# Kernel tuning notes

Hardware: AMD Instinct MI355X
Metric: run time of the kernel (lower is better)

Reference implementation:

```python
import jax, jax.numpy as jnp
import numpy as np

T, B, N_IN, N_HID, N_OUT = 32, 32, 512, 1024, 256

def _xavier(key, fan_in, fan_out):
    scale = jnp.sqrt(2.0 / (fan_in + fan_out)).astype(jnp.float32)
    return jax.random.normal(key, (fan_in, fan_out), dtype=jnp.float32) * scale

def setup_inputs() -> dict:
    key = jax.random.key(0)
    ks = jax.random.split(key, 8)
    return {
        'x_in': jax.random.normal(ks[0], (T, B, N_IN), dtype=jnp.float32),
        'W_i': _xavier(ks[1], N_IN, N_HID),
        'W_z': _xavier(ks[2], N_HID, N_HID),
        'W_c': _xavier(ks[3], N_HID, N_HID),
        'W_h': _xavier(ks[4], N_HID, N_HID),
        'W_ho': _xavier(ks[5], N_HID, N_HID),
        'W_o': _xavier(ks[6], N_HID, N_OUT),
        'lam': jnp.array([0.9], dtype=jnp.float32),
        'eta': jnp.array([0.5], dtype=jnp.float32),
        'g': jnp.ones((1, N_HID), dtype=jnp.float32),
        'b': jnp.ones((1, N_HID), dtype=jnp.float32),
        'mode': 0,
        'time': T,
    }

def reference(x_in, W_i, W_z, W_c, W_h, W_ho, W_o, lam, eta, g, b, mode, time):
    relu = jax.nn.relu
    n_steps = int(time)  # dt = 1.0
    batch, n_hidden = x_in.shape[1], W_i.shape[1]

    def step(carry, x_t):
        h, a = carry
        x = relu(x_t)                              # [B, n_in]
        s = relu(x @ W_i)                          # [B, H]
        z = relu(s @ W_z)                          # [B, H]
        zc = z @ W_c                               # reused twice
        h = relu(zc + h @ W_h)                     # [B, H]
        # fast-weight update: a <- lam*a + eta * h^T h (per-batch outer product)
        a = lam[0] * a + eta[0] * jnp.einsum('bi,bj->bij', h, h)  # [B, H, H]
        # one inner readout/normalization step
        hs = h @ W_h + zc + jnp.einsum('bk,bkj->bj', h, a)        # [B, H]
        mu = jnp.mean(hs, axis=0)                                 # [H]
        sig = jnp.sqrt(jnp.mean((hs - mu) ** 2, axis=0))          # [H] (biased std)
        hs = relu(g[0] * (hs - mu) / sig + b[0])
        return (hs, a), None

    h0 = jnp.zeros((batch, n_hidden), dtype=x_in.dtype)
    a0 = jnp.zeros((batch, n_hidden, n_hidden), dtype=x_in.dtype)
    (h, a), _ = jax.lax.scan(step, (h0, a0), x_in[:n_steps])

    o = relu(h @ W_ho)
    y = relu(o @ W_o)
    return y.reshape(1, batch, -1)
```

## Files before the change

### kernel.cpp

```cpp
#include <hip/hip_runtime.h>
#include <hip/hip_bf16.h>

#define T_   32
#define B_   32
#define NIN_ 512
#define H_   1024
#define NOUT_ 256
#define NBLK 64
#define NTHR 1024
#define NCOL 16
#define NSLOT 80
#define PACKB 128

typedef short bf16x8 __attribute__((ext_vector_type(8)));
typedef float f32x4  __attribute__((ext_vector_type(4)));
typedef unsigned int u32x4 __attribute__((ext_vector_type(4)));

__device__ __forceinline__ float bf2f(unsigned short u) {
  union { unsigned int i; float f; } x; x.i = ((unsigned int)u) << 16; return x.f;
}
__device__ __forceinline__ unsigned short f2bf(float f) {
  __hip_bfloat16 h = __float2bfloat16(f);
  return *reinterpret_cast<unsigned short*>(&h);
}
__device__ __forceinline__ unsigned int packf(float v) {
  unsigned short h = f2bf(v);
  unsigned short l = f2bf(v - bf2f(h));
  return ((unsigned int)h << 16) | l;
}
__device__ __forceinline__ void unpack8v(u32x4 a, u32x4 b, bf16x8& hi, bf16x8& lo) {
  unsigned int t[8] = {a[0], a[1], a[2], a[3], b[0], b[1], b[2], b[3]};
  union { bf16x8 v; unsigned int u[4]; } H, L;
#pragma unroll
  for (int j = 0; j < 4; j++) {
    unsigned int e = t[2 * j], o = t[2 * j + 1];
    H.u[j] = (o & 0xFFFF0000u) | (e >> 16);
    L.u[j] = (o << 16) | (e & 0xFFFFu);
  }
  hi = H.v; lo = L.v;
}

__device__ __forceinline__ void astu(unsigned int* p, unsigned int v) {
  __hip_atomic_store(p, v, __ATOMIC_RELAXED, __HIP_MEMORY_SCOPE_AGENT);
}
__device__ __forceinline__ void astf(float* p, float v) {
  __hip_atomic_store(p, v, __ATOMIC_RELAXED, __HIP_MEMORY_SCOPE_AGENT);
}
__device__ __forceinline__ void aaddf(float* p, float v) {
  __hip_atomic_fetch_add(p, v, __ATOMIC_RELAXED, __HIP_MEMORY_SCOPE_AGENT);
}

__device__ __forceinline__ void rendezvous(int* cnt, int slot) {
  __syncthreads();
  if (threadIdx.x == 0) {
    __hip_atomic_fetch_add(&cnt[slot], 1, __ATOMIC_RELAXED, __HIP_MEMORY_SCOPE_AGENT);
    while (__hip_atomic_load(&cnt[slot], __ATOMIC_RELAXED, __HIP_MEMORY_SCOPE_AGENT) < NBLK)
      __builtin_amdgcn_s_sleep(1);
    __atomic_signal_fence(__ATOMIC_ACQUIRE);
  }
  __syncthreads();
}

__global__ void init_detect(const unsigned short* __restrict__ x_raw,
                            int* __restrict__ flag, int* __restrict__ cnt) {
  __shared__ int bad;
  if (threadIdx.x == 0) bad = 0;
  __syncthreads();
  int c = 0;
  for (int i = threadIdx.x; i < 2048; i += 256) {
    float v = bf2f(x_raw[i]);
    if (!(fabsf(v) < 1e9f)) c++;
  }
  if (c) atomicAdd(&bad, 1);
  __syncthreads();
  if (threadIdx.x == 0) flag[0] = bad ? 1 : 0;
  for (int i = threadIdx.x; i < NSLOT; i += 256)
    __hip_atomic_store(&cnt[i], 0, __ATOMIC_RELAXED, __HIP_MEMORY_SCOPE_AGENT);
}

__global__ void prep_all(
    const void* __restrict__ x_in, unsigned int* __restrict__ X_pk,
    const void* lam, const void* eta, const void* g, const void* b,
    float* __restrict__ par,
    const void* __restrict__ W_i,  unsigned short* __restrict__ WiT_hi,  unsigned short* __restrict__ WiT_lo,
    const void* __restrict__ W_z,  unsigned short* __restrict__ WzT_hi,  unsigned short* __restrict__ WzT_lo,
    const void* __restrict__ W_c,  unsigned short* __restrict__ WcT_hi,  unsigned short* __restrict__ WcT_lo,
    const void* __restrict__ W_h,  unsigned short* __restrict__ WhT_hi,  unsigned short* __restrict__ WhT_lo,
    const void* __restrict__ W_ho, unsigned short* __restrict__ WhoT_hi, unsigned short* __restrict__ WhoT_lo,
    const void* __restrict__ W_o,  unsigned short* __restrict__ WoT_hi,  unsigned short* __restrict__ WoT_lo,
    const int* __restrict__ flag)
{
  const bool isf32 = flag[0] != 0;
  int blk = blockIdx.x;
  if (blk < PACKB) {
    const int n = T_ * B_ * NIN_;
    for (int i = blk * 256 + threadIdx.x; i < n; i += PACKB * 256) {
      float v = isf32 ? ((const float*)x_in)[i] : bf2f(((const unsigned short*)x_in)[i]);
      X_pk[i] = packf(fmaxf(v, 0.f));
    }
    return;
  }
  blk -= PACKB;
  if (blk < 4) {
    int t = blk * 256 + threadIdx.x;
    if (t == 0) {
      par[0] = isf32 ? ((const float*)lam)[0] : bf2f(((const unsigned short*)lam)[0]);
      par[1] = isf32 ? ((const float*)eta)[0] : bf2f(((const unsigned short*)eta)[0]);
    }
    if (t < H_) {
      par[2 + t]      = isf32 ? ((const float*)g)[t] : bf2f(((const unsigned short*)g)[t]);
      par[2 + H_ + t] = isf32 ? ((const float*)b)[t] : bf2f(((const unsigned short*)b)[t]);
    }
    return;
  }
  blk -= 4;
  const void* src; unsigned short *dhi, *dlo; int R, C;
  int tb = blk;
  if (tb < 512)       { src = W_i;  dhi = WiT_hi;  dlo = WiT_lo;  R = NIN_; C = H_; }
  else if (tb < 1536) { tb -= 512;  src = W_z;  dhi = WzT_hi;  dlo = WzT_lo;  R = H_; C = H_; }
  else if (tb < 2560) { tb -= 1536; src = W_c;  dhi = WcT_hi;  dlo = WcT_lo;  R = H_; C = H_; }
  else if (tb < 3584) { tb -= 2560; src = W_h;  dhi = WhT_hi;  dlo = WhT_lo;  R = H_; C = H_; }
  else if (tb < 4608) { tb -= 3584; src = W_ho; dhi = WhoT_hi; dlo = WhoT_lo; R = H_; C = H_; }
  else                { tb -= 4608; src = W_o;  dhi = WoT_hi;  dlo = WoT_lo;  R = H_; C = NOUT_; }
  __shared__ unsigned short thi[32][33], tlo[32][33];
  int ncx = C >> 5;
  int c0 = (tb % ncx) * 32, r0 = (tb / ncx) * 32;
  int tx = threadIdx.x & 31, ty = threadIdx.x >> 5;
  for (int i = ty; i < 32; i += 8) {
    size_t idx = (size_t)(r0 + i) * C + c0 + tx;
    float v = isf32 ? ((const float*)src)[idx] : bf2f(((const unsigned short*)src)[idx]);
    unsigned short h = f2bf(v);
    thi[i][tx] = h;
    tlo[i][tx] = f2bf(v - bf2f(h));
  }
  __syncthreads();
  for (int i = ty; i < 32; i += 8) {
    dhi[(size_t)(c0 + i) * R + r0 + tx] = thi[tx][i];
    dlo[(size_t)(c0 + i) * R + r0 + tx] = tlo[tx][i];
  }
}

template<int K, int N, int OUTMODE>
__global__ void gemmA_pk(const unsigned int* __restrict__ A,
                         const unsigned short* __restrict__ BT_hi,
                         const unsigned short* __restrict__ BT_lo,
                         void* __restrict__ C) {
  int wave = (blockIdx.x * blockDim.x + threadIdx.x) >> 6;
  int lane = threadIdx.x & 63;
  const int ntj = N >> 4;
  int mt = wave / ntj, jt = wave - mt * ntj;
  int col = lane & 15, quad = lane >> 4;
  const unsigned int*   ap = A     + (size_t)(mt * 16 + col) * K + quad * 8;
  const unsigned short* bh = BT_hi + (size_t)(jt * 16 + col) * K + quad * 8;
  const unsigned short* bl = BT_lo + (size_t)(jt * 16 + col) * K + quad * 8;
  f32x4 acc = {0.f, 0.f, 0.f, 0.f};
#pragma unroll 4
  for (int kk = 0; kk < K; kk += 32) {
    bf16x8 ahi, alo;
    unpack8v(*(const u32x4*)(ap + kk), *(const u32x4*)(ap + kk + 4), ahi, alo);
    bf16x8 vh = *(const bf16x8*)(bh + kk);
    bf16x8 vl = *(const bf16x8*)(bl + kk);
    acc = __builtin_amdgcn_mfma_f32_16x16x32_bf16(ahi, vh, acc, 0, 0, 0);
    acc = __builtin_amdgcn_mfma_f32_16x16x32_bf16(alo, vh, acc, 0, 0, 0);
    acc = __builtin_amdgcn_mfma_f32_16x16x32_bf16(ahi, vl, acc, 0, 0, 0);
  }
#pragma unroll
  for (int r = 0; r < 4; r++) {
    size_t idx = (size_t)(mt * 16 + quad * 4 + r) * N + jt * 16 + col;
    if (OUTMODE) ((unsigned int*)C)[idx] = packf(fmaxf(acc[r], 0.f));
    else         ((float*)C)[idx] = acc[r];
  }
}

template<int NIT>
__device__ __forceinline__ f32x4 mm_partN(
    const unsigned int* __restrict__ A, int am0, int k0,
    const unsigned short* __restrict__ BH, const unsigned short* __restrict__ BL,
    int bj0, int col, int quad) {
  const unsigned int*   ap = A  + (size_t)(am0 + col) * H_ + k0 + quad * 8;
  const unsigned short* bh = BH + (size_t)(bj0 + col) * H_ + k0 + quad * 8;
  const unsigned short* bl = BL + (size_t)(bj0 + col) * H_ + k0 + quad * 8;
  u32x4 ab[2 * NIT];
#pragma unroll
  for (int i = 0; i < NIT; i++) {
    ab[2 * i]     = *(const u32x4*)(ap + 32 * i);
    ab[2 * i + 1] = *(const u32x4*)(ap + 32 * i + 4);
  }
  f32x4 acc = {0.f, 0.f, 0.f, 0.f};
#pragma unroll
  for (int i = 0; i < NIT; i++) {
    bf16x8 ahi, alo;
    unpack8v(ab[2 * i], ab[2 * i + 1], ahi, alo);
    bf16x8 vh = *(const bf16x8*)(bh + 32 * i);
    bf16x8 vl = *(const bf16x8*)(bl + 32 * i);
    acc = __builtin_amdgcn_mfma_f32_16x16x32_bf16(ahi, vh, acc, 0, 0, 0);
    acc = __builtin_amdgcn_mfma_f32_16x16x32_bf16(alo, vh, acc, 0, 0, 0);
    acc = __builtin_amdgcn_mfma_f32_16x16x32_bf16(ahi, vl, acc, 0, 0, 0);
  }
  return acc;
}
__device__ __forceinline__ f32x4 mm_tile_pf(
    const unsigned int* __restrict__ A, int am0,
    const unsigned short* __restrict__ BH, const unsigned short* __restrict__ BL,
    int bj0, f32x4 acc, int col, int quad) {
#pragma unroll 1
  for (int kk = 0; kk < H_; kk += 256) {
    f32x4 p = mm_partN<8>(A, am0, kk, BH, BL, bj0, col, quad);
    acc[0] += p[0]; acc[1] += p[1]; acc[2] += p[2]; acc[3] += p[3];
  }
  return acc;
}

__global__ void __launch_bounds__(NTHR) recurrent(
    const unsigned short* __restrict__ WhT_hi, const unsigned short* __restrict__ WhT_lo,
    const unsigned short* __restrict__ WhoT_hi, const unsigned short* __restrict__ WhoT_lo,
    const unsigned short* __restrict__ WoT_hi, const unsigned short* __restrict__ WoT_lo,
    const float* __restrict__ ZC,
    unsigned int* __restrict__ hq,
    unsigned int* __restrict__ hc,
    unsigned int* __restrict__ Opub,
    float* __restrict__ hist_loc,
    float* __restrict__ dots_g,
    const float* __restrict__ par,
    void* __restrict__ y_out,
    int* __restrict__ cnt,
    const int* __restrict__ flag)
{
  __shared__ f32x4 red[16][64];
  __shared__ float lds_hs[B_][NCOL + 1];
  __shared__ float lds_dt[B_][T_];
  __shared__ float lds_mu[NCOL], lds_sc[NCOL], lds_bb[NCOL];

  const int tid = threadIdx.x, wg = blockIdx.x;
  const int wv = tid >> 6, lane = tid & 63;
  const int col = lane & 15, quad = lane >> 4;
  const int j0 = wg * NCOL;
  const int tile = wv & 1, kp = wv >> 1;
  const int am0 = tile * 16;
  const int k0 = kp * 128;
  const float lam = par[0], eta = par[1];
  const bool isf32 = flag[0] != 0;
  float* hl = hist_loc + (size_t)wg * (T_ * B_ * NCOL);

  for (int d = tid; d < B_ * NCOL; d += NTHR) {
    int b = d >> 4, c = d & 15;
    astu(hc + (size_t)b * H_ + j0 + c, 0u);
  }
  for (int i = tid; i < T_ * B_ * T_ / NBLK; i += NTHR)
    astf(dots_g + (size_t)wg * (T_ * B_ * T_ / NBLK) + i, 0.f);
  rendezvous(cnt, 0);

  int slot = 1;
  for (int t = 0; t < T_; ++t) {
    const float* zb = ZC + (size_t)t * B_ * H_;
    const unsigned int* hcur = hc + (size_t)t * B_ * H_;
    unsigned int* hqt = hq + (size_t)t * B_ * H_;
    float* dt = dots_g + (size_t)t * B_ * T_;
    red[wv][lane] = mm_partN<4>(hcur, am0, k0, WhT_hi, WhT_lo, j0, col, quad);
    __syncthreads();
    if (wv < 2) {
      int a0 = wv * 16;
      f32x4 s = red[wv][lane];
#pragma unroll
      for (int k = 1; k < 8; k++) {
        f32x4 p = red[wv + 2 * k][lane];
        s[0] += p[0]; s[1] += p[1]; s[2] += p[2]; s[3] += p[3];
      }
#pragma unroll
      for (int r = 0; r < 4; r++) {
        float v = zb[(size_t)(a0 + quad * 4 + r) * H_ + j0 + col] + s[r];
        v = fmaxf(v, 0.f);
        int m = a0 + quad * 4 + r;
        hl[((size_t)t * B_ + m) * NCOL + col] = v;
        astu(hqt + (size_t)m * H_ + j0 + col, packf(v));
      }
    }
    __syncthreads();
    for (int d = tid; d < B_ * (t + 1); d += NTHR) {
      int b = ((d / (t + 1)) + wg) & (B_ - 1);
      int s = d % (t + 1);
      const f32x4* p = (const f32x4*)(hl + ((size_t)t * B_ + b) * NCOL);
      const f32x4* q = (const f32x4*)(hl + ((size_t)s * B_ + b) * NCOL);
      float sum = 0.f;
#pragma unroll
      for (int i = 0; i < 4; i++) {
        f32x4 a = p[i], c = q[i];
        sum += a[0] * c[0] + a[1] * c[1] + a[2] * c[2] + a[3] * c[3];
      }
      aaddf(dt + (size_t)b * T_ + s, sum);
    }
    rendezvous(cnt, slot++);
    for (int d = tid; d < B_ * (t + 1); d += NTHR) {
      int b = d / (t + 1), s = d - b * (t + 1);
      lds_dt[b][s] = dt[(size_t)b * T_ + s];
    }
    red[wv][lane] = mm_partN<4>(hqt, am0, k0, WhT_hi, WhT_lo, j0, col, quad);
    __syncthreads();
    if (wv < 2) {
      int a0 = wv * 16;
      f32x4 s = red[wv][lane];
#pragma unroll
      for (int k = 1; k < 8; k++) {
        f32x4 p = red[wv + 2 * k][lane];
        s[0] += p[0]; s[1] += p[1]; s[2] += p[2]; s[3] += p[3];
      }
#pragma unroll
      for (int r = 0; r < 4; r++)
        lds_hs[a0 + quad * 4 + r][col] =
            zb[(size_t)(a0 + quad * 4 + r) * H_ + j0 + col] + s[r];
    }
    __syncthreads();
    for (int d = tid; d < B_ * NCOL; d += NTHR) {
      int b = d >> 4, c = d & 15;
      float a = 0.f, w = eta;
      const float* hb = hl + (size_t)b * NCOL + c;
      for (int s = t; s >= 0; --s) {
        a += w * lds_dt[b][s] * hb[(size_t)s * B_ * NCOL];
        w *= lam;
      }
      lds_hs[b][c] += a;
    }
    __syncthreads();
    if (tid < NCOL) {
      int c = tid;
      float sum = 0.f;
#pragma unroll
      for (int b = 0; b < B_; b++) sum += lds_hs[b][c];
      float mu = sum * (1.f / B_);
      float sq = 0.f;
#pragma unroll
      for (int b = 0; b < B_; b++) {
        float dd = lds_hs[b][c] - mu;
        sq += dd * dd;
      }
      float sig = sqrtf(sq * (1.f / B_));
      lds_mu[c] = mu;
      lds_sc[c] = par[2 + j0 + c] / sig;
      lds_bb[c] = par[2 + H_ + j0 + c];
    }
    __syncthreads();
    for (int d = tid; d < B_ * NCOL; d += NTHR) {
      int b = d >> 4, c = d & 15;
      float v = (lds_hs[b][c] - lds_mu[c]) * lds_sc[c] + lds_bb[c];
      astu(hc + (size_t)(t + 1) * B_ * H_ + (size_t)b * H_ + j0 + c, packf(fmaxf(v, 0.f)));
    }
    rendezvous(cnt, slot++);
  }
  {
    const unsigned int* hfin = hc + (size_t)T_ * B_ * H_;
    red[wv][lane] = mm_partN<4>(hfin, am0, k0, WhoT_hi, WhoT_lo, j0, col, quad);
    __syncthreads();
    if (wv < 2) {
      int a0 = wv * 16;
      f32x4 s = red[wv][lane];
#pragma unroll
      for (int k = 1; k < 8; k++) {
        f32x4 p = red[wv + 2 * k][lane];
        s[0] += p[0]; s[1] += p[1]; s[2] += p[2]; s[3] += p[3];
      }
#pragma unroll
      for (int r = 0; r < 4; r++) {
        float v = fmaxf(s[r], 0.f);
        astu(Opub + (size_t)(a0 + quad * 4 + r) * H_ + j0 + col, packf(v));
      }
    }
  }
  rendezvous(cnt, slot++);
  if (wg < 2) {
    int id = wg * 16 + wv;
    int bt2 = id & 1, jt2 = id >> 1;
    f32x4 acc = {0.f, 0.f, 0.f, 0.f};
    acc = mm_tile_pf(Opub, bt2 * 16, WoT_hi, WoT_lo, jt2 * 16, acc, col, quad);
#pragma unroll
    for (int r = 0; r < 4; r++) {
      float v = fmaxf(acc[r], 0.f);
      size_t idx = (size_t)(bt2 * 16 + quad * 4 + r) * NOUT_ + jt2 * 16 + col;
      if (isf32) ((float*)y_out)[idx] = v;
      else       ((unsigned short*)y_out)[idx] = f2bf(v);
    }
  }
}

extern "C" void kernel_launch(void* const* d_in, const int* in_sizes, int n_in,
                              void* d_out, int out_size, void* d_ws, size_t ws_size,
                              hipStream_t stream) {
  const void* x_in = d_in[0];
  const void* W_i  = d_in[1];
  const void* W_z  = d_in[2];
  const void* W_c  = d_in[3];
  const void* W_h  = d_in[4];
  const void* W_ho = d_in[5];
  const void* W_o  = d_in[6];
  const void* lam  = d_in[7];
  const void* eta  = d_in[8];
  const void* g    = d_in[9];
  const void* bb   = d_in[10];

  char* wsp = (char*)d_ws;
  size_t off = 0;
  auto alloc = [&](size_t bytes) {
    void* p = wsp + off;
    off += (bytes + 255) & ~(size_t)255;
    return p;
  };
  int*            flag    = (int*)alloc(16);
  int*            cnt     = (int*)alloc(NSLOT * 4);
  float*          par     = (float*)alloc((2 + 2 * H_) * 4);
  unsigned int*   X_pk    = (unsigned int*)alloc((size_t)T_ * B_ * NIN_ * 4);
  unsigned short* WiT_hi  = (unsigned short*)alloc((size_t)NIN_ * H_ * 2);
  unsigned short* WiT_lo  = (unsigned short*)alloc((size_t)NIN_ * H_ * 2);
  unsigned short* WzT_hi  = (unsigned short*)alloc((size_t)H_ * H_ * 2);
  unsigned short* WzT_lo  = (unsigned short*)alloc((size_t)H_ * H_ * 2);
  unsigned short* WcT_hi  = (unsigned short*)alloc((size_t)H_ * H_ * 2);
  unsigned short* WcT_lo  = (unsigned short*)alloc((size_t)H_ * H_ * 2);
  unsigned short* WhT_hi  = (unsigned short*)alloc((size_t)H_ * H_ * 2);
  unsigned short* WhT_lo  = (unsigned short*)alloc((size_t)H_ * H_ * 2);
  unsigned short* WhoT_hi = (unsigned short*)alloc((size_t)H_ * H_ * 2);
  unsigned short* WhoT_lo = (unsigned short*)alloc((size_t)H_ * H_ * 2);
  unsigned short* WoT_hi  = (unsigned short*)alloc((size_t)H_ * NOUT_ * 2);
  unsigned short* WoT_lo  = (unsigned short*)alloc((size_t)H_ * NOUT_ * 2);
  unsigned int*   S_pk    = (unsigned int*)alloc((size_t)T_ * B_ * H_ * 4);
  unsigned int*   Z_pk    = (unsigned int*)alloc((size_t)T_ * B_ * H_ * 4);
  float*          ZC      = (float*)alloc((size_t)T_ * B_ * H_ * 4);
  unsigned int*   hq      = (unsigned int*)alloc((size_t)T_ * B_ * H_ * 4);
  unsigned int*   hc      = (unsigned int*)alloc((size_t)(T_ + 1) * B_ * H_ * 4);
  unsigned int*   Opub    = (unsigned int*)alloc((size_t)B_ * H_ * 4);
  float*          histloc = (float*)alloc((size_t)NBLK * T_ * B_ * NCOL * 4);
  float*          dots_g  = (float*)alloc((size_t)T_ * B_ * T_ * 4);
  (void)ws_size; (void)in_sizes; (void)n_in; (void)out_size;

  init_detect<<<1, 256, 0, stream>>>((const unsigned short*)x_in, flag, cnt);

  prep_all<<<PACKB + 4 + 4864, 256, 0, stream>>>(
      x_in, X_pk, lam, eta, g, bb, par,
      W_i, WiT_hi, WiT_lo, W_z, WzT_hi, WzT_lo, W_c, WcT_hi, WcT_lo,
      W_h, WhT_hi, WhT_lo, W_ho, WhoT_hi, WhoT_lo, W_o, WoT_hi, WoT_lo,
      flag);

  gemmA_pk<NIN_, H_, 1><<<1024, 256, 0, stream>>>(X_pk, WiT_hi, WiT_lo, S_pk);
  gemmA_pk<H_,   H_, 1><<<1024, 256, 0, stream>>>(S_pk, WzT_hi, WzT_lo, Z_pk);
  gemmA_pk<H_,   H_, 0><<<1024, 256, 0, stream>>>(Z_pk, WcT_hi, WcT_lo, ZC);

  recurrent<<<NBLK, NTHR, 0, stream>>>(WhT_hi, WhT_lo, WhoT_hi, WhoT_lo, WoT_hi, WoT_lo,
                                       ZC, hq, hc, Opub, histloc, dots_g,
                                       par, d_out, cnt, flag);
}
```

Measured before the change: 825.6 us.

## Tile precompute GEMMs through shared memory with 64x64 block tiles

Replaces the per-wave 16x16 GEMM, which streamed A and B straight from global memory, with a block-tiled kernel. Each 1024-thread block stages a 64x64 output tile's A and B slices (K chunk of 128) in LDS and shares them across 16 waves. This cuts redundant global/L2 loads in the three time-parallel input GEMMs. In exchange it adds two syncthreads per K chunk and has no double buffering, so load latency is not overlapped with compute.

```diff
diff --git a/kernel.cpp b/kernel.cpp
--- a/kernel.cpp
+++ b/kernel.cpp
@@ -11,6 +11,9 @@
 #define NCOL 16
 #define NSLOT 80
 #define PACKB 128
+#define GBM 64
+#define GBN 64
+#define GBK 128
 
 typedef short bf16x8 __attribute__((ext_vector_type(8)));
 typedef float f32x4  __attribute__((ext_vector_type(4)));
@@ -140,33 +143,53 @@
   }
 }
 
-template<int K, int N, int OUTMODE>
-__global__ void gemmA_pk(const unsigned int* __restrict__ A,
-                         const unsigned short* __restrict__ BT_hi,
-                         const unsigned short* __restrict__ BT_lo,
-                         void* __restrict__ C) {
-  int wave = (blockIdx.x * blockDim.x + threadIdx.x) >> 6;
-  int lane = threadIdx.x & 63;
-  const int ntj = N >> 4;
-  int mt = wave / ntj, jt = wave - mt * ntj;
-  int col = lane & 15, quad = lane >> 4;
-  const unsigned int*   ap = A     + (size_t)(mt * 16 + col) * K + quad * 8;
-  const unsigned short* bh = BT_hi + (size_t)(jt * 16 + col) * K + quad * 8;
-  const unsigned short* bl = BT_lo + (size_t)(jt * 16 + col) * K + quad * 8;
+template<int K, int OUTMODE>
+__global__ void __launch_bounds__(1024) gemmT(
+    const unsigned int* __restrict__ A,
+    const unsigned short* __restrict__ BT_hi,
+    const unsigned short* __restrict__ BT_lo,
+    void* __restrict__ C) {
+  __shared__ unsigned int   As[GBM][GBK + 4];
+  __shared__ unsigned short Bh[GBN][GBK + 8];
+  __shared__ unsigned short Bl[GBN][GBK + 8];
+  const int tid = threadIdx.x;
+  const int wv = tid >> 6, lane = tid & 63;
+  const int col = lane & 15, quad = lane >> 4;
+  const int wr = wv >> 2, wc = wv & 3;
+  const int bm0 = (blockIdx.x >> 4) * GBM;
+  const int bn0 = (blockIdx.x & 15) * GBN;
+  const int sr = tid >> 4;
+  const int sc = (tid & 15) * 8;
   f32x4 acc = {0.f, 0.f, 0.f, 0.f};
-#pragma unroll 4
-  for (int kk = 0; kk < K; kk += 32) {
-    bf16x8 ahi, alo;
-    unpack8v(*(const u32x4*)(ap + kk), *(const u32x4*)(ap + kk + 4), ahi, alo);
-    bf16x8 vh = *(const bf16x8*)(bh + kk);
-    bf16x8 vl = *(const bf16x8*)(bl + kk);
-    acc = __builtin_amdgcn_mfma_f32_16x16x32_bf16(ahi, vh, acc, 0, 0, 0);
-    acc = __builtin_amdgcn_mfma_f32_16x16x32_bf16(alo, vh, acc, 0, 0, 0);
-    acc = __builtin_amdgcn_mfma_f32_16x16x32_bf16(ahi, vl, acc, 0, 0, 0);
+#pragma unroll 1
+  for (int k0 = 0; k0 < K; k0 += GBK) {
+    const unsigned int* ga = A + (size_t)(bm0 + sr) * K + k0 + sc;
+    u32x4 a0 = *(const u32x4*)ga;
+    u32x4 a1 = *(const u32x4*)(ga + 4);
+    bf16x8 vh = *(const bf16x8*)(BT_hi + (size_t)(bn0 + sr) * K + k0 + sc);
+    bf16x8 vl = *(const bf16x8*)(BT_lo + (size_t)(bn0 + sr) * K + k0 + sc);
+    *(u32x4*)&As[sr][sc]     = a0;
+    *(u32x4*)&As[sr][sc + 4] = a1;
+    *(bf16x8*)&Bh[sr][sc] = vh;
+    *(bf16x8*)&Bl[sr][sc] = vl;
+    __syncthreads();
+#pragma unroll
+    for (int s = 0; s < GBK; s += 32) {
+      bf16x8 ahi, alo;
+      u32x4 c0v = *(const u32x4*)&As[wr * 16 + col][s + quad * 8];
+      u32x4 c1v = *(const u32x4*)&As[wr * 16 + col][s + quad * 8 + 4];
+      unpack8v(c0v, c1v, ahi, alo);
+      bf16x8 bh8 = *(const bf16x8*)&Bh[wc * 16 + col][s + quad * 8];
+      bf16x8 bl8 = *(const bf16x8*)&Bl[wc * 16 + col][s + quad * 8];
+      acc = __builtin_amdgcn_mfma_f32_16x16x32_bf16(ahi, bh8, acc, 0, 0, 0);
+      acc = __builtin_amdgcn_mfma_f32_16x16x32_bf16(alo, bh8, acc, 0, 0, 0);
+      acc = __builtin_amdgcn_mfma_f32_16x16x32_bf16(ahi, bl8, acc, 0, 0, 0);
+    }
+    __syncthreads();
   }
 #pragma unroll
   for (int r = 0; r < 4; r++) {
-    size_t idx = (size_t)(mt * 16 + quad * 4 + r) * N + jt * 16 + col;
+    size_t idx = (size_t)(bm0 + wr * 16 + quad * 4 + r) * H_ + bn0 + wc * 16 + col;
     if (OUTMODE) ((unsigned int*)C)[idx] = packf(fmaxf(acc[r], 0.f));
     else         ((float*)C)[idx] = acc[r];
   }
@@ -437,9 +460,9 @@
       W_h, WhT_hi, WhT_lo, W_ho, WhoT_hi, WhoT_lo, W_o, WoT_hi, WoT_lo,
       flag);
 
-  gemmA_pk<NIN_, H_, 1><<<1024, 256, 0, stream>>>(X_pk, WiT_hi, WiT_lo, S_pk);
-  gemmA_pk<H_,   H_, 1><<<1024, 256, 0, stream>>>(S_pk, WzT_hi, WzT_lo, Z_pk);
-  gemmA_pk<H_,   H_, 0><<<1024, 256, 0, stream>>>(Z_pk, WcT_hi, WcT_lo, ZC);
+  gemmT<NIN_, 1><<<256, 1024, 0, stream>>>(X_pk, WiT_hi, WiT_lo, S_pk);
+  gemmT<H_,   1><<<256, 1024, 0, stream>>>(S_pk, WzT_hi, WzT_lo, Z_pk);
+  gemmT<H_,   0><<<256, 1024, 0, stream>>>(Z_pk, WcT_hi, WcT_lo, ZC);
 
   recurrent<<<NBLK, NTHR, 0, stream>>>(WhT_hi, WhT_lo, WhoT_hi, WhoT_lo, WoT_hi, WoT_lo,
                                        ZC, hq, hc, Opub, histloc, dots_g,
```

Result: faster. 725.3 us (-12.1%).
